# Kernel optimization log

Hardware: AMD Instinct MI355X
Metric: run time of the kernel (lower is better)

The kernel has to match this reference:

```python
import jax, jax.numpy as jnp
import numpy as np

NEG_INF = -1e9


def setup_inputs() -> dict:
    key = jax.random.key(0)
    ks = jax.random.split(key, 7)
    N, Q, C = 16, 4096, 77
    D, Dc, H, S = 512, 768, 8, 64
    scale = 0.02
    return {
        "query": jax.random.normal(ks[0], (N, Q, D), jnp.float32),
        "context": jax.random.normal(ks[1], (N, C, Dc), jnp.float32),
        "Wq": jax.random.normal(ks[2], (D, H, S), jnp.float32) * scale,
        "Wk": jax.random.normal(ks[3], (Dc, H, S), jnp.float32) * scale,
        "Wv": jax.random.normal(ks[4], (Dc, H, S), jnp.float32) * scale,
        "Wo": jax.random.normal(ks[5], (H, S, D), jnp.float32) * scale,
        "bo": jnp.zeros((D,), jnp.float32),
    }


def reference(query, context, Wq, Wk, Wv, Wo, bo):
    # Projections: split hidden dim into heads.
    q = jnp.einsum('NQD,DHS->NQHS', query, Wq)      # [N,Q,H,S]
    k = jnp.einsum('NCD,DHS->NCHS', context, Wk)    # [N,C,H,S]
    v = jnp.einsum('NCD,DHS->NCHS', context, Wv)    # [N,C,H,S]
    size_per_head = q.shape[-1]
    # Attention scores [N,H,Q,C], scaled by 1/sqrt(S).
    scores = jnp.einsum('NQHS,NCHS->NHQC', q, k) * (size_per_head ** -0.5)
    weights = jax.nn.softmax(scores, axis=3)
    out = jnp.einsum('NHQC,NCHS->NQHS', weights, v)  # [N,Q,H,S]
    # Merge heads back to model dim with output bias.
    return jnp.einsum('NQHS,HSD->NQD', out, Wo) + bo
```

## Files before the change

kernel.cpp:

```cpp
#include <hip/hip_runtime.h>

typedef unsigned short u16;
typedef unsigned int u32;
typedef __bf16 bf16_t;
typedef bf16_t bf16x8 __attribute__((ext_vector_type(8)));
typedef float floatx4 __attribute__((ext_vector_type(4)));

__device__ __forceinline__ float bf2f(u16 h) {
    union { unsigned u; float f; } v;
    v.u = ((unsigned)h) << 16;
    return v.f;
}

__device__ __forceinline__ u16 f2bf(float f) {
    union { float f; unsigned u; } v;
    v.f = f;
    unsigned r = v.u + 0x7fffu + ((v.u >> 16) & 1u);
    return (u16)(r >> 16);
}

typedef __attribute__((address_space(1))) const u32 gu32;
typedef __attribute__((address_space(3))) u32 lu32;
__device__ __forceinline__ void gload16(const void* g, void* l) {
    __builtin_amdgcn_global_load_lds((gu32*)g, (lu32*)l, 16, 0, 0);
}

__global__ void transpose_one(const float* __restrict__ W, u16* __restrict__ Wt,
                              int K, int N) {
    int idx = blockIdx.x * 256 + threadIdx.x;
    if (idx >= K * N) return;
    int nrow = idx / K;
    int k = idx - nrow * K;
    Wt[idx] = f2bf(W[k * N + nrow]);
}

__global__ void transpose_kv(const float* __restrict__ Wk, const float* __restrict__ Wv,
                             u16* __restrict__ Wt) {
    int idx = blockIdx.x * 256 + threadIdx.x;
    if (idx >= 1024 * 768) return;
    int nrow = idx / 768;
    int k = idx - nrow * 768;
    Wt[idx] = f2bf((nrow < 512) ? Wk[k * 512 + nrow] : Wv[k * 512 + (nrow - 512)]);
}

__global__ void transpose_v(const u16* __restrict__ kv, u16* __restrict__ vt) {
    int idx = blockIdx.x * 256 + threadIdx.x;
    if (idx >= 16 * 8 * 64 * 96) return;
    int c  = idx % 96;
    int t1 = idx / 96;
    int s  = t1 & 63;
    int t2 = t1 >> 6;
    int h  = t2 & 7;
    int n  = t2 >> 3;
    u16 val = 0;
    if (c < 77) val = kv[((long)(n * 77 + c)) * 1024 + 512 + h * 64 + s];
    vt[idx] = val;
}

#define TM 128
#define TN 256
#define TK 32

template <bool A_F32, bool OUT_F32>
__global__ __launch_bounds__(512, 4) void gemm_bt(
    const void* __restrict__ A_, const u16* __restrict__ Bt,
    void* __restrict__ C_, const float* __restrict__ bias,
    int M, int K, int N, int ntl2)
{
    constexpr int AB = A_F32 ? TM * TK * 4 : TM * TK * 2;
    constexpr int BB = TN * TK * 2;
    __shared__ __align__(16) char smem[2 * (AB + BB)];

    const int tid  = threadIdx.x;
    const int lane = tid & 63;
    const int wave = tid >> 6;
    const int quad = lane >> 4;
    const int l16  = lane & 15;
    const int wm   = (wave & 1) * 64;
    const int wn   = (wave >> 1) * 64;

    const int nwg = gridDim.x;
    const int wg  = blockIdx.x;
    const int t   = (wg & 7) * (nwg >> 3) + (wg >> 3);
    const long bm = (long)(t >> ntl2) * TM;
    const long bn = (long)(t & ((1 << ntl2) - 1)) * TN;

    const float* Af = (const float*)A_;
    const u16*   Ab = (const u16*)A_;

    floatx4 acc[4][4] = {};

    auto stage = [&](int b, int k0) {
        char* Abase = smem + b * (AB + BB);
        u16*  Bb    = (u16*)(Abase + AB);
        #pragma unroll
        for (int p = 0; p < 2; ++p) {
            int ch  = p * 512 + tid;
            int row = ch >> 2;
            int pc  = ch & 3;
            gload16(Bt + (bn + row) * K + k0 + pc * 8,
                    Bb + (p * 512 + wave * 64) * 8);
        }
        if (A_F32) {
            #pragma unroll
            for (int p = 0; p < 2; ++p) {
                int ch  = p * 512 + tid;
                int row = ch >> 3;
                int pcs = (ch & 7) ^ (row & 7);
                long gr = bm + row;
                if (gr < M)
                    gload16(Af + gr * K + k0 + pcs * 4,
                            (float*)Abase + (p * 512 + wave * 64) * 4);
            }
        } else {
            int row = tid >> 2;
            int pc  = tid & 3;
            long gr = bm + row;
            if (gr < M)
                gload16(Ab + gr * K + k0 + pc * 8,
                        (u16*)Abase + (wave * 64) * 8);
        }
    };

    const int nk = K / TK;
    stage(0, 0);
    __syncthreads();

    for (int tt = 0; tt < nk; ++tt) {
        const int cb = tt & 1;
        if (tt + 1 < nk) stage(cb ^ 1, (tt + 1) * TK);

        const char* Abase = smem + cb * (AB + BB);
        const u16*  Bb    = (const u16*)(Abase + AB);

        bf16x8 af[4], bfr[4];
        #pragma unroll
        for (int i = 0; i < 4; ++i) {
            int row = wm + i * 16 + l16;
            if (A_F32) {
                const char* arow = Abase + (size_t)row * 128;
                int x = row & 7;
                float4 f0 = *(const float4*)(arow + (((quad * 2)     ^ x) * 16));
                float4 f1 = *(const float4*)(arow + (((quad * 2 + 1) ^ x) * 16));
                union { bf16_t h[8]; bf16x8 v; } pk;
                pk.h[0] = (bf16_t)f0.x; pk.h[1] = (bf16_t)f0.y;
                pk.h[2] = (bf16_t)f0.z; pk.h[3] = (bf16_t)f0.w;
                pk.h[4] = (bf16_t)f1.x; pk.h[5] = (bf16_t)f1.y;
                pk.h[6] = (bf16_t)f1.z; pk.h[7] = (bf16_t)f1.w;
                af[i] = pk.v;
            } else {
                af[i] = *(const bf16x8*)((const u16*)Abase + row * 32 + quad * 8);
            }
        }
        #pragma unroll
        for (int j = 0; j < 4; ++j)
            bfr[j] = *(const bf16x8*)(Bb + (wn + j * 16 + l16) * 32 + quad * 8);
        #pragma unroll
        for (int i = 0; i < 4; ++i)
            #pragma unroll
            for (int j = 0; j < 4; ++j)
                acc[i][j] = __builtin_amdgcn_mfma_f32_16x16x32_bf16(
                    af[i], bfr[j], acc[i][j], 0, 0, 0);

        __syncthreads();
    }

    #pragma unroll
    for (int i = 0; i < 4; ++i) {
        #pragma unroll
        for (int r = 0; r < 4; ++r) {
            long row = bm + wm + i * 16 + quad * 4 + r;
            if (row >= M) continue;
            #pragma unroll
            for (int j = 0; j < 4; ++j) {
                long col = bn + wn + j * 16 + l16;
                float val = acc[i][j][r];
                if (bias) val += bias[col];
                if (OUT_F32) ((float*)C_)[row * N + col] = val;
                else         ((u16*)C_)[row * N + col] = f2bf(val);
            }
        }
    }
}

__global__ __launch_bounds__(256) void attn_kernel(
    const u16* __restrict__ qb,
    const u16* __restrict__ kvb,
    const u16* __restrict__ vt,
    u16* __restrict__ ob)
{
    const int QL = 4096, HS = 512;
    const int q0 = blockIdx.x * 256;
    const int h  = blockIdx.y;
    const int n  = blockIdx.z;

    __shared__ u16 sQP[128 * 104];
    __shared__ u16 ks [80 * 72];
    __shared__ u16 vts[64 * 104];

    const int tid  = threadIdx.x;
    const int lane = tid & 63;
    const int wave = tid >> 6;
    const int quad = lane >> 4;
    const int l16  = lane & 15;
    const int wm   = wave * 32;

    const u16* kbase = kvb + (long)n * 77 * 1024 + h * 64;
    for (int v = tid; v < 640; v += 256) {
        int c = v >> 3, g = (v & 7) * 8;
        uint4 val = make_uint4(0, 0, 0, 0);
        if (c < 77) val = *(const uint4*)(kbase + (long)c * 1024 + g);
        *(uint4*)(&ks[c * 72 + g]) = val;
    }
    const u16* vtbase = vt + (long)((n * 8 + h) * 64) * 96;
    for (int v = tid; v < 768; v += 256) {
        int r = v / 12, c8 = v - r * 12;
        *(uint4*)(&vts[r * 104 + c8 * 8]) = *(const uint4*)(vtbase + v * 8);
    }
    __syncthreads();

    const bool v4ok = (l16 < 13);

    for (int it = 0; it < 2; ++it) {
        const long qrow0 = (long)q0 + it * 128;
        const u16* qbase = qb + ((long)n * QL + qrow0) * HS + h * 64;
        u16*       obase = ob + ((long)n * QL + qrow0) * HS + h * 64;

        #pragma unroll
        for (int p = 0; p < 4; ++p) {
            int v = tid + p * 256;
            int r = v >> 3, g = (v & 7) * 8;
            *(uint4*)(&sQP[r * 72 + g]) = *(const uint4*)(qbase + (long)r * HS + g);
        }
        __syncthreads();

        floatx4 accS[2][5] = {};
        #pragma unroll
        for (int kk = 0; kk < 2; ++kk) {
            bf16x8 aq[2], bk[5];
            #pragma unroll
            for (int t = 0; t < 2; ++t)
                aq[t] = *(const bf16x8*)(&sQP[(wm + t * 16 + l16) * 72 + kk * 32 + quad * 8]);
            #pragma unroll
            for (int j = 0; j < 5; ++j)
                bk[j] = *(const bf16x8*)(&ks[(j * 16 + l16) * 72 + kk * 32 + quad * 8]);
            #pragma unroll
            for (int t = 0; t < 2; ++t)
                #pragma unroll
                for (int j = 0; j < 5; ++j)
                    accS[t][j] = __builtin_amdgcn_mfma_f32_16x16x32_bf16(
                        aq[t], bk[j], accS[t][j], 0, 0, 0);
        }

        float pw[2][5][4];
        #pragma unroll
        for (int t = 0; t < 2; ++t) {
            #pragma unroll
            for (int r = 0; r < 4; ++r) {
                float v0 = accS[t][0][r] * 0.125f;
                float v1 = accS[t][1][r] * 0.125f;
                float v2 = accS[t][2][r] * 0.125f;
                float v3 = accS[t][3][r] * 0.125f;
                float v4 = v4ok ? accS[t][4][r] * 0.125f : -1e30f;
                float mx = fmaxf(fmaxf(fmaxf(v0, v1), fmaxf(v2, v3)), v4);
                mx = fmaxf(mx, __shfl_xor(mx, 1));
                mx = fmaxf(mx, __shfl_xor(mx, 2));
                mx = fmaxf(mx, __shfl_xor(mx, 4));
                mx = fmaxf(mx, __shfl_xor(mx, 8));
                float e0 = __expf(v0 - mx), e1 = __expf(v1 - mx);
                float e2 = __expf(v2 - mx), e3 = __expf(v3 - mx);
                float e4 = __expf(v4 - mx);
                float sum = e0 + e1 + e2 + e3 + e4;
                sum += __shfl_xor(sum, 1);
                sum += __shfl_xor(sum, 2);
                sum += __shfl_xor(sum, 4);
                sum += __shfl_xor(sum, 8);
                float inv = 1.f / sum;
                pw[t][0][r] = e0 * inv; pw[t][1][r] = e1 * inv;
                pw[t][2][r] = e2 * inv; pw[t][3][r] = e3 * inv;
                pw[t][4][r] = e4 * inv;
            }
        }
        __syncthreads();

        #pragma unroll
        for (int t = 0; t < 2; ++t) {
            #pragma unroll
            for (int r = 0; r < 4; ++r) {
                int row = wm + t * 16 + quad * 4 + r;
                #pragma unroll
                for (int j = 0; j < 5; ++j)
                    sQP[row * 104 + j * 16 + l16] = f2bf(pw[t][j][r]);
                sQP[row * 104 + 80 + l16] = 0;
            }
        }
        __syncthreads();

        floatx4 accO[2][4] = {};
        #pragma unroll
        for (int kk = 0; kk < 3; ++kk) {
            bf16x8 aw[2], bv[4];
            #pragma unroll
            for (int t = 0; t < 2; ++t)
                aw[t] = *(const bf16x8*)(&sQP[(wm + t * 16 + l16) * 104 + kk * 32 + quad * 8]);
            #pragma unroll
            for (int j = 0; j < 4; ++j)
                bv[j] = *(const bf16x8*)(&vts[(j * 16 + l16) * 104 + kk * 32 + quad * 8]);
            #pragma unroll
            for (int t = 0; t < 2; ++t)
                #pragma unroll
                for (int j = 0; j < 4; ++j)
                    accO[t][j] = __builtin_amdgcn_mfma_f32_16x16x32_bf16(
                        aw[t], bv[j], accO[t][j], 0, 0, 0);
        }

        #pragma unroll
        for (int t = 0; t < 2; ++t)
            #pragma unroll
            for (int j = 0; j < 4; ++j)
                #pragma unroll
                for (int r = 0; r < 4; ++r) {
                    int row = wm + t * 16 + quad * 4 + r;
                    obase[(long)row * HS + j * 16 + l16] = f2bf(accO[t][j][r]);
                }
        __syncthreads();
    }
}

extern "C" void kernel_launch(void* const* d_in, const int* in_sizes, int n_in,
                              void* d_out, int out_size, void* d_ws, size_t ws_size,
                              hipStream_t stream) {
    const float* query   = (const float*)d_in[0];
    const float* context = (const float*)d_in[1];
    const float* Wq      = (const float*)d_in[2];
    const float* Wk      = (const float*)d_in[3];
    const float* Wv      = (const float*)d_in[4];
    const float* Wo      = (const float*)d_in[5];
    const float* bo      = (const float*)d_in[6];
    float* out = (float*)d_out;

    u16* q_ws  = (u16*)d_ws;
    u16* kv_ws = q_ws + 33554432;
    u16* WqT   = kv_ws + 1261568;
    u16* WkvT  = WqT + 262144;
    u16* WoT   = WkvT + 786432;
    u16* vt_ws = WkvT;

    transpose_one<<<(512 * 512 + 255) / 256, 256, 0, stream>>>(Wq, WqT, 512, 512);
    transpose_kv<<<(1024 * 768 + 255) / 256, 256, 0, stream>>>(Wk, Wv, WkvT);
    transpose_one<<<(512 * 512 + 255) / 256, 256, 0, stream>>>(Wo, WoT, 512, 512);

    gemm_bt<true, false><<<dim3(1024), 512, 0, stream>>>(
        (const void*)query, WqT, (void*)q_ws, nullptr, 65536, 512, 512, 1);
    gemm_bt<true, false><<<dim3(40), 512, 0, stream>>>(
        (const void*)context, WkvT, (void*)kv_ws, nullptr, 1232, 768, 1024, 2);
    transpose_v<<<(16 * 8 * 64 * 96 + 255) / 256, 256, 0, stream>>>(kv_ws, vt_ws);
    attn_kernel<<<dim3(16, 8, 16), 256, 0, stream>>>(q_ws, kv_ws, vt_ws, q_ws);
    gemm_bt<false, true><<<dim3(1024), 512, 0, stream>>>(
        (const void*)q_ws, WoT, (void*)out, bo, 65536, 512, 512, 1);
}
```

Measured before the change: 424.7 us.

## XOR-swizzle bf16 LDS tiles and overlap prefetch with explicit vmcnt waits

Applies an XOR swizzle to the bf16 A and B tiles in LDS, reducing bank conflicts on the 16-byte fragment reads. Replaces __syncthreads with explicit s_waitcnt vmcnt counts plus raw barriers, so the next stage's global-to-LDS loads stay in flight during the current MFMA step. Row bounds checks become clamping to the last row, removing divergent branches around the async loads. The hand-tuned vmcnt values must match the exact number of issued loads, or the kernel can read stale LDS data.

```diff
diff --git a/kernel.cpp b/kernel.cpp
--- a/kernel.cpp
+++ b/kernel.cpp
@@ -87,6 +87,7 @@
 
     const float* Af = (const float*)A_;
     const u16*   Ab = (const u16*)A_;
+    const long   Mm1 = (long)M - 1;
 
     floatx4 acc[4][4] = {};
 
@@ -97,7 +98,7 @@
         for (int p = 0; p < 2; ++p) {
             int ch  = p * 512 + tid;
             int row = ch >> 2;
-            int pc  = ch & 3;
+            int pc  = (ch & 3) ^ ((row >> 1) & 3);
             gload16(Bt + (bn + row) * K + k0 + pc * 8,
                     Bb + (p * 512 + wave * 64) * 8);
         }
@@ -107,28 +108,33 @@
                 int ch  = p * 512 + tid;
                 int row = ch >> 3;
                 int pcs = (ch & 7) ^ (row & 7);
-                long gr = bm + row;
-                if (gr < M)
-                    gload16(Af + gr * K + k0 + pcs * 4,
-                            (float*)Abase + (p * 512 + wave * 64) * 4);
+                long gr = bm + row; if (gr > Mm1) gr = Mm1;
+                gload16(Af + gr * K + k0 + pcs * 4,
+                        (float*)Abase + (p * 512 + wave * 64) * 4);
             }
         } else {
             int row = tid >> 2;
-            int pc  = tid & 3;
-            long gr = bm + row;
-            if (gr < M)
-                gload16(Ab + gr * K + k0 + pc * 8,
-                        (u16*)Abase + (wave * 64) * 8);
+            int pc  = (tid & 3) ^ ((row >> 1) & 3);
+            long gr = bm + row; if (gr > Mm1) gr = Mm1;
+            gload16(Ab + gr * K + k0 + pc * 8,
+                    (u16*)Abase + (wave * 64) * 8);
         }
     };
 
     const int nk = K / TK;
     stage(0, 0);
-    __syncthreads();
 
     for (int tt = 0; tt < nk; ++tt) {
         const int cb = tt & 1;
-        if (tt + 1 < nk) stage(cb ^ 1, (tt + 1) * TK);
+        if (tt + 1 < nk) {
+            stage(cb ^ 1, (tt + 1) * TK);
+            if (A_F32) asm volatile("s_waitcnt vmcnt(4)" ::: "memory");
+            else       asm volatile("s_waitcnt vmcnt(3)" ::: "memory");
+        } else {
+            asm volatile("s_waitcnt vmcnt(0)" ::: "memory");
+        }
+        __builtin_amdgcn_s_barrier();
+        __builtin_amdgcn_sched_barrier(0);
 
         const char* Abase = smem + cb * (AB + BB);
         const u16*  Bb    = (const u16*)(Abase + AB);
@@ -149,12 +155,16 @@
                 pk.h[6] = (bf16_t)f1.z; pk.h[7] = (bf16_t)f1.w;
                 af[i] = pk.v;
             } else {
-                af[i] = *(const bf16x8*)((const u16*)Abase + row * 32 + quad * 8);
-            }
-        }
-        #pragma unroll
-        for (int j = 0; j < 4; ++j)
-            bfr[j] = *(const bf16x8*)(Bb + (wn + j * 16 + l16) * 32 + quad * 8);
+                int pcs = quad ^ ((row >> 1) & 3);
+                af[i] = *(const bf16x8*)((const u16*)Abase + row * 32 + pcs * 8);
+            }
+        }
+        #pragma unroll
+        for (int j = 0; j < 4; ++j) {
+            int row = wn + j * 16 + l16;
+            int pcs = quad ^ ((row >> 1) & 3);
+            bfr[j] = *(const bf16x8*)(Bb + row * 32 + pcs * 8);
+        }
         #pragma unroll
         for (int i = 0; i < 4; ++i)
             #pragma unroll
@@ -162,7 +172,7 @@
                 acc[i][j] = __builtin_amdgcn_mfma_f32_16x16x32_bf16(
                     af[i], bfr[j], acc[i][j], 0, 0, 0);
 
-        __syncthreads();
+        __builtin_amdgcn_s_barrier();
     }
 
     #pragma unroll
```

Result: no change. 419.3 us (-1.3%).
